# Performance work log

Measured on AMD Instinct MI355X. Metric: run time of the kernel, lower is better.

## Reference

```python
import jax, jax.numpy as jnp
import numpy as np

D_VOCAB, D_MODEL, N_CTX, D_MLP, D_HEAD, N_HEADS, N_LAYERS = 32000, 1024, 2048, 4096, 64, 16, 4
BATCH, SEQ = 2, 2048


def setup_inputs() -> dict:
    key = jax.random.key(0)
    ks = jax.random.split(key, 12)
    sd = 1.0 / np.sqrt(D_MODEL)
    inp = {
        'tokens': jax.random.randint(ks[0], (BATCH, SEQ), 0, D_VOCAB),
        'W_E': jax.random.normal(ks[1], (D_MODEL, D_VOCAB), jnp.float32) * sd,
        'W_pos': jax.random.normal(ks[2], (N_CTX, D_MODEL), jnp.float32) * sd,
        'W_K': jax.random.normal(ks[3], (N_LAYERS, N_HEADS, D_HEAD, D_MODEL), jnp.float32) * sd,
        'W_Q': jax.random.normal(ks[4], (N_LAYERS, N_HEADS, D_HEAD, D_MODEL), jnp.float32) * sd,
        'W_V': jax.random.normal(ks[5], (N_LAYERS, N_HEADS, D_HEAD, D_MODEL), jnp.float32) * sd,
        'W_O': jax.random.normal(ks[6], (N_LAYERS, D_MODEL, D_HEAD * N_HEADS), jnp.float32) * sd,
        'W_in': jax.random.normal(ks[7], (N_LAYERS, D_MLP, D_MODEL), jnp.float32) * sd,
        'b_in': jnp.zeros((N_LAYERS, D_MLP), jnp.float32),
        'W_out': jax.random.normal(ks[8], (N_LAYERS, D_MODEL, D_MLP), jnp.float32) * sd,
        'b_out': jnp.zeros((N_LAYERS, D_MODEL), jnp.float32),
        'W_U': jax.random.normal(ks[9], (D_MODEL, D_VOCAB), jnp.float32) / np.sqrt(D_VOCAB),
    }
    return inp


def reference(tokens, W_E, W_pos, W_K, W_Q, W_V, W_O, W_in, b_in, W_out, b_out, W_U):
    P = tokens.shape[-1]
    # Embed: einsum('dbp->bpd', W_E[:, x])  ==  W_E.T[tokens]
    x = W_E.T[tokens]                      # [b, p, d]
    x = x + W_pos[:P]                      # PosEmbed
    causal = jnp.tril(jnp.ones((P, P), dtype=bool))  # mask[q, p]: p <= q
    scale = 1.0 / np.sqrt(D_HEAD)
    for l in range(N_LAYERS):
        # --- Attention ---
        k = jnp.einsum('ihd,bpd->biph', W_K[l], x)
        q = jnp.einsum('ihd,bpd->biph', W_Q[l], x)
        v = jnp.einsum('ihd,bpd->biph', W_V[l], x)
        scores = jnp.einsum('biph,biqh->biqp', k, q)
        # tril(scores) - 1e10*(1-mask)  ==  where(mask, scores, -1e10)
        masked = jnp.where(causal, scores, jnp.float32(-1e10))
        attn = jax.nn.softmax(masked * scale, axis=-1)   # softmax over keys p
        z = jnp.einsum('biph,biqp->biqh', v, attn)       # [b, i, q, h]
        z_flat = jnp.transpose(z, (0, 2, 1, 3)).reshape(z.shape[0], P, -1)  # b q (i h)
        attn_out = jnp.einsum('df,bqf->bqd', W_O[l], z_flat)
        x = x + attn_out
        # --- MLP (ReLU) ---
        pre = jnp.einsum('md,bpd->bpm', W_in[l], x) + b_in[l]
        post = jax.nn.relu(pre)
        x = x + jnp.einsum('dm,bpm->bpd', W_out[l], post) + b_out[l]
    return x @ W_U                          # logits [b, p, d_vocab]
```

## Files before the change

### kernel.cpp

```cpp
#include <hip/hip_runtime.h>
#include <hip/hip_bf16.h>
#include <math.h>

#define DV   32000
#define DM   1024
#define DMLP 4096
#define DH   64
#define NH   16
#define NL   4
#define BATCH 2
#define S    2048
#define MTOK (BATCH*S)

typedef __bf16 bf16_t;
typedef bf16_t bf16x8 __attribute__((ext_vector_type(8)));
typedef float  f32x4  __attribute__((ext_vector_type(4)));

#define AS1 __attribute__((address_space(1)))
#define AS3 __attribute__((address_space(3)))

__device__ __forceinline__ void gload16(const bf16_t* g, bf16_t* l) {
    __builtin_amdgcn_global_load_lds((const AS1 void*)g, (AS3 void*)l, 16, 0, 0);
}

__device__ __forceinline__ unsigned short bfbits(float v) {
    union { bf16_t b; unsigned short u; } c; c.b = (bf16_t)v; return c.u;
}
__device__ __forceinline__ float b2f(unsigned short u) {
    union { float f; unsigned v; } c; c.v = ((unsigned)u) << 16; return c.f;
}

template<int MODE, bool BIAS, bool RELU>
__global__ __launch_bounds__(256, 2)
void gemm128d(const bf16_t* __restrict__ A, const bf16_t* __restrict__ Bm,
              char* __restrict__ Out, int ldc,
              const float* __restrict__ bias,
              float* __restrict__ resid, bf16_t* __restrict__ residb,
              int K)
{
    const int mb = blockIdx.x, nb = blockIdx.y;

    __shared__ alignas(16) bf16_t lds[2][2][128*64];

    const int tid  = threadIdx.x;
    const int wave = tid >> 6, lane = tid & 63;
    const int wm = wave >> 1, wn = wave & 1;
    const int l16 = lane & 15, lh = lane >> 4;

    const bf16_t* Abase = A  + (long)(mb*128)*K;
    const bf16_t* Bbase = Bm + (long)(nb*128)*K;

    auto stage = [&](int buf, int mat, int k0) {
        const bf16_t* src = (mat ? Bbase : Abase) + k0;
        bf16_t* dst = &lds[buf][mat][0];
#pragma unroll
        for (int u=0; u<4; ++u) {
            int c = u*256 + tid;
            int row = c >> 3, lc = (c & 7) ^ (row & 7);
            gload16(&src[(long)row*K + lc*8], dst + c*8);
        }
    };

    f32x4 acc[4][4];
#pragma unroll
    for (int i=0;i<4;i++)
#pragma unroll
        for (int j=0;j<4;j++) { f32x4 zv={0.f,0.f,0.f,0.f}; acc[i][j]=zv; }

    const int NT = K >> 6;
    stage(0,0,0); stage(0,1,0);

    int cur = 0;
    for (int kt = 0; kt < NT; ++kt) {
        const int nxt = cur ^ 1;
        const int k1 = (kt+1) << 6;
        const bool more = (kt+1 < NT);

        if (more) {
            stage(nxt,0,k1);
            asm volatile("s_waitcnt vmcnt(4)" ::: "memory");
        } else {
            asm volatile("s_waitcnt vmcnt(0)" ::: "memory");
        }
        asm volatile("s_barrier" ::: "memory");

        bf16x8 af[4][2], bfr[4][2];
#pragma unroll
        for (int i=0;i<4;i++) {
            int ra = wm*64 + i*16 + l16;
#pragma unroll
            for (int kk=0;kk<2;kk++)
                af[i][kk] = *(const bf16x8*)&lds[cur][0][ra*64 + (((kk*4+lh)^(ra&7))*8)];
        }
#pragma unroll
        for (int j=0;j<2;j++) {
            int rb = wn*64 + j*16 + l16;
#pragma unroll
            for (int kk=0;kk<2;kk++)
                bfr[j][kk] = *(const bf16x8*)&lds[cur][1][rb*64 + (((kk*4+lh)^(rb&7))*8)];
        }
        __builtin_amdgcn_s_setprio(1);
#pragma unroll
        for (int kk=0;kk<2;kk++)
#pragma unroll
            for (int i=0;i<4;i++)
#pragma unroll
                for (int j=0;j<2;j++)
                    acc[i][j] = __builtin_amdgcn_mfma_f32_16x16x32_bf16(af[i][kk], bfr[j][kk], acc[i][j], 0,0,0);
        __builtin_amdgcn_s_setprio(0);

        if (more) stage(nxt,1,k1);
#pragma unroll
        for (int j=2;j<4;j++) {
            int rb = wn*64 + j*16 + l16;
#pragma unroll
            for (int kk=0;kk<2;kk++)
                bfr[j][kk] = *(const bf16x8*)&lds[cur][1][rb*64 + (((kk*4+lh)^(rb&7))*8)];
        }
        __builtin_amdgcn_s_setprio(1);
#pragma unroll
        for (int kk=0;kk<2;kk++)
#pragma unroll
            for (int i=0;i<4;i++)
#pragma unroll
                for (int j=2;j<4;j++)
                    acc[i][j] = __builtin_amdgcn_mfma_f32_16x16x32_bf16(af[i][kk], bfr[j][kk], acc[i][j], 0,0,0);
        __builtin_amdgcn_s_setprio(0);

        asm volatile("s_barrier" ::: "memory");
        cur = nxt;
    }

    if constexpr (MODE == 1) {
        float* lsl = reinterpret_cast<float*>(&lds[0][0][0]) + wave*(32*68);
        const int lrow = lane >> 4;
        const int lcq  = lane & 15;
#pragma unroll
        for (int ch=0; ch<2; ++ch) {
#pragma unroll
            for (int il=0; il<2; ++il)
#pragma unroll
                for (int j=0;j<4;j++)
#pragma unroll
                    for (int r=0;r<4;r++)
                        lsl[(il*16 + lh*4 + r)*68 + j*16 + l16] = acc[ch*2+il][j][r];
#pragma unroll
            for (int u=0; u<8; ++u) {
                int rl = u*4 + lrow;
                f32x4 v = *(const f32x4*)&lsl[rl*68 + lcq*4];
                long row = mb*128 + wm*64 + ch*32 + rl;
                long col = nb*128 + wn*64 + lcq*4;
                __builtin_nontemporal_store(v, (f32x4*)&((float*)Out)[row*ldc + col]);
            }
        }
    } else {
#pragma unroll
        for (int i=0;i<4;i++) {
            int row0 = mb*128 + wm*64 + i*16 + lh*4;
#pragma unroll
            for (int j=0;j<4;j++) {
                int col = nb*128 + wn*64 + j*16 + l16;
                float bv = BIAS ? bias[col] : 0.0f;
#pragma unroll
                for (int r=0;r<4;r++) {
                    int row = row0 + r;
                    float v = acc[i][j][r] + bv;
                    if (RELU) v = v > 0.f ? v : 0.f;
                    if constexpr (MODE == 0) {
                        ((bf16_t*)Out)[(long)row*ldc + col] = (bf16_t)v;
                    } else {
                        long o2 = (long)row*ldc + col;
                        float nv = resid[o2] + v;
                        resid[o2]  = nv;
                        residb[o2] = (bf16_t)nv;
                    }
                }
            }
        }
    }
}

template<int MODE, bool BIAS, bool RELU>
__global__ __launch_bounds__(512, 1)
void gemm256(const bf16_t* __restrict__ A, const bf16_t* __restrict__ Bm,
             char* __restrict__ Out, int ldc,
             const float* __restrict__ bias, int K)
{
    const int mb = blockIdx.x, nb = blockIdx.y;

    __shared__ alignas(16) bf16_t lds[2][2][2][128*64];

    const int tid  = threadIdx.x;
    const int wave = tid >> 6, lane = tid & 63;
    const int wm = wave >> 2, wn = wave & 3;
    const int l16 = lane & 15, lh = lane >> 4;

    const bf16_t* Abase = A  + (long)(mb*256)*K;
    const bf16_t* Bbase = Bm + (long)(nb*256)*K;

    const int c0 = tid,       r0 = c0 >> 3, lc0 = (c0 & 7) ^ (r0 & 7);
    const int c1 = 512 + tid, r1 = c1 >> 3, lc1 = (c1 & 7) ^ (r1 & 7);

    auto stage = [&](int buf, int mat, int half, int k0) {
        const bf16_t* src = (mat ? Bbase : Abase) + (long)(half*128)*K + k0;
        bf16_t* dst = &lds[buf][mat][half][0];
        gload16(&src[(long)r0*K + lc0*8], dst + c0*8);
        gload16(&src[(long)r1*K + lc1*8], dst + c1*8);
    };

    f32x4 acc[8][4];
#pragma unroll
    for (int i=0;i<8;i++)
#pragma unroll
        for (int j=0;j<4;j++) { f32x4 zv={0.f,0.f,0.f,0.f}; acc[i][j]=zv; }

    const int NT = K >> 6;
    stage(0,0,0,0); stage(0,0,1,0); stage(0,1,0,0); stage(0,1,1,0);

    int cur = 0;
    for (int kt = 0; kt < NT; ++kt) {
        const int nxt = cur ^ 1;
        const int k1 = (kt+1) << 6;
        const bool more = (kt+1 < NT);

        if (more) {
            stage(nxt,0,0,k1);
            asm volatile("s_waitcnt vmcnt(2)" ::: "memory");
        } else {
            asm volatile("s_waitcnt vmcnt(0)" ::: "memory");
        }
        asm volatile("s_barrier" ::: "memory");

        bf16x8 af[4][2], bfr[4][2];
#pragma unroll
        for (int i=0;i<4;i++) {
            int ra = i*16 + l16;
#pragma unroll
            for (int kk=0;kk<2;kk++)
                af[i][kk] = *(const bf16x8*)&lds[cur][0][wm][ra*64 + (((kk*4+lh)^(ra&7))*8)];
        }
#pragma unroll
        for (int j=0;j<2;j++) {
            int rb = (wn&1)*64 + j*16 + l16;
#pragma unroll
            for (int kk=0;kk<2;kk++)
                bfr[j][kk] = *(const bf16x8*)&lds[cur][1][wn>>1][rb*64 + (((kk*4+lh)^(rb&7))*8)];
        }
        __builtin_amdgcn_s_setprio(1);
#pragma unroll
        for (int kk=0;kk<2;kk++)
#pragma unroll
            for (int i=0;i<4;i++)
#pragma unroll
                for (int j=0;j<2;j++)
                    acc[i][j] = __builtin_amdgcn_mfma_f32_16x16x32_bf16(af[i][kk], bfr[j][kk], acc[i][j], 0,0,0);
        __builtin_amdgcn_s_setprio(0);

        if (more) stage(nxt,0,1,k1);
#pragma unroll
        for (int j=2;j<4;j++) {
            int rb = (wn&1)*64 + j*16 + l16;
#pragma unroll
            for (int kk=0;kk<2;kk++)
                bfr[j][kk] = *(const bf16x8*)&lds[cur][1][wn>>1][rb*64 + (((kk*4+lh)^(rb&7))*8)];
        }
        __builtin_amdgcn_s_setprio(1);
#pragma unroll
        for (int kk=0;kk<2;kk++)
#pragma unroll
            for (int i=0;i<4;i++)
#pragma unroll
                for (int j=2;j<4;j++)
                    acc[i][j] = __builtin_amdgcn_mfma_f32_16x16x32_bf16(af[i][kk], bfr[j][kk], acc[i][j], 0,0,0);
        __builtin_amdgcn_s_setprio(0);

        if (more) stage(nxt,1,0,k1);
#pragma unroll
        for (int i=0;i<4;i++) {
            int ra = (i+4)*16 + l16;
#pragma unroll
            for (int kk=0;kk<2;kk++)
                af[i][kk] = *(const bf16x8*)&lds[cur][0][wm][ra*64 + (((kk*4+lh)^(ra&7))*8)];
        }
        __builtin_amdgcn_s_setprio(1);
#pragma unroll
        for (int kk=0;kk<2;kk++)
#pragma unroll
            for (int i=0;i<4;i++)
#pragma unroll
                for (int j=0;j<2;j++)
                    acc[i+4][j] = __builtin_amdgcn_mfma_f32_16x16x32_bf16(af[i][kk], bfr[j][kk], acc[i+4][j], 0,0,0);
        __builtin_amdgcn_s_setprio(0);

        if (more) stage(nxt,1,1,k1);
        __builtin_amdgcn_s_setprio(1);
#pragma unroll
        for (int kk=0;kk<2;kk++)
#pragma unroll
            for (int i=0;i<4;i++)
#pragma unroll
                for (int j=2;j<4;j++)
                    acc[i+4][j] = __builtin_amdgcn_mfma_f32_16x16x32_bf16(af[i][kk], bfr[j][kk], acc[i+4][j], 0,0,0);
        __builtin_amdgcn_s_setprio(0);

        asm volatile("s_barrier" ::: "memory");
        cur = nxt;
    }

#pragma unroll
    for (int i=0;i<8;i++) {
        int row0 = mb*256 + wm*128 + i*16 + lh*4;
#pragma unroll
        for (int j=0;j<4;j++) {
            int col = nb*256 + wn*64 + j*16 + l16;
            float bv = BIAS ? bias[col] : 0.0f;
#pragma unroll
            for (int r=0;r<4;r++) {
                int row = row0 + r;
                float v = acc[i][j][r] + bv;
                if (RELU) v = v > 0.f ? v : 0.f;
                ((bf16_t*)Out)[(long)row*ldc + col] = (bf16_t)v;
            }
        }
    }
}

__global__ __launch_bounds__(256)
void flash_attn(const bf16_t* __restrict__ qkvf,
                const bf16_t* __restrict__ vtg,
                bf16_t* __restrict__ zf)
{
    const int qt = blockIdx.x;
    const int bh = blockIdx.y;
    const int b  = bh >> 4, hd = bh & 15;

    __shared__ alignas(16) bf16_t Kl[64*64];
    __shared__ alignas(16) bf16_t Vtl[64*64];
    __shared__ alignas(16) bf16_t Pl[4*32*64];

    const int tid = threadIdx.x;
    const int wave = tid >> 6, lane = tid & 63;
    const int l16 = lane & 15, lh = lane >> 4;
    const int wq_lo = qt*128 + wave*32;
    bf16_t* Pw = Pl + wave*32*64;

    bf16x8 qr[2][2];
#pragma unroll
    for (int qf=0; qf<2; qf++) {
        int qg = wq_lo + qf*16 + l16;
#pragma unroll
        for (int dhh=0; dhh<2; dhh++)
            qr[qf][dhh] = *(const bf16x8*)&qkvf[((long)b*S + qg)*3072 + hd*64 + dhh*32 + lh*8];
    }

    f32x4 o[4][2];
#pragma unroll
    for (int d=0; d<4; d++)
#pragma unroll
        for (int qf=0; qf<2; qf++) { f32x4 zv={0.f,0.f,0.f,0.f}; o[d][qf]=zv; }
    float mrun[2] = {-1e30f, -1e30f};
    float lrun[2] = {0.f, 0.f};

    const int nt = 2*(qt+1);
    const float C = 0.125f;

    for (int t = 0; t < nt; ++t) {
        const int kv0 = t*64;
        __syncthreads();
#pragma unroll
        for (int u=0; u<2; ++u) {
            int c = u*256 + tid;
            int row = c >> 3, lc = (c & 7) ^ (row & 7);
            gload16(&qkvf[((long)b*S + kv0 + row)*3072 + 1024 + hd*64 + lc*8], &Kl[c*8]);
        }
#pragma unroll
        for (int u=0; u<2; ++u) {
            int c = u*256 + tid;
            int row = c >> 3, lc = (c & 7) ^ (row & 7);
            gload16(&vtg[((long)bh*DH + row)*S + kv0 + lc*8], &Vtl[c*8]);
        }
        __syncthreads();

        f32x4 s[4][2];
#pragma unroll
        for (int f=0; f<4; f++)
#pragma unroll
            for (int qf=0; qf<2; qf++) { f32x4 zv={0.f,0.f,0.f,0.f}; s[f][qf]=zv; }
        __builtin_amdgcn_s_setprio(1);
#pragma unroll
        for (int f=0; f<4; f++) {
            int krow = f*16 + l16;
#pragma unroll
            for (int dhh=0; dhh<2; dhh++) {
                bf16x8 kfr = *(const bf16x8*)&Kl[krow*64 + (((dhh*4+lh) ^ (krow&7))*8)];
#pragma unroll
                for (int qf=0; qf<2; qf++)
                    s[f][qf] = __builtin_amdgcn_mfma_f32_16x16x32_bf16(kfr, qr[qf][dhh], s[f][qf], 0,0,0);
            }
        }
        __builtin_amdgcn_s_setprio(0);

        const bool needmask = (kv0 + 64 > wq_lo);

#pragma unroll
        for (int qf=0; qf<2; qf++) {
            int qg = wq_lo + qf*16 + l16;
            float pmax = -1e30f;
#pragma unroll
            for (int f=0; f<4; f++)
#pragma unroll
                for (int r=0; r<4; r++) {
                    float sv = s[f][qf][r];
                    if (needmask && (kv0 + f*16 + lh*4 + r > qg)) { sv = -1e30f; s[f][qf][r] = sv; }
                    pmax = fmaxf(pmax, sv);
                }
            pmax = fmaxf(pmax, __shfl_xor(pmax, 16));
            pmax = fmaxf(pmax, __shfl_xor(pmax, 32));
            float mnew = fmaxf(mrun[qf], pmax);
            float corr = __expf((mrun[qf] - mnew)*C);
            mrun[qf] = mnew;
            lrun[qf] *= corr;
#pragma unroll
            for (int d=0; d<4; d++) o[d][qf] *= corr;
            float lsum = 0.f;
            int qloc = qf*16 + l16;
#pragma unroll
            for (int f=0; f<4; f++) {
                ushort4 pk;
                float p0 = __expf((s[f][qf][0]-mnew)*C);
                float p1 = __expf((s[f][qf][1]-mnew)*C);
                float p2 = __expf((s[f][qf][2]-mnew)*C);
                float p3 = __expf((s[f][qf][3]-mnew)*C);
                lsum += (p0+p1) + (p2+p3);
                pk.x = bfbits(p0); pk.y = bfbits(p1); pk.z = bfbits(p2); pk.w = bfbits(p3);
                int phys = (f*2 + (lh>>1)) ^ (qloc & 7);
                *(ushort4*)&Pw[qloc*64 + phys*8 + (lh&1)*4] = pk;
            }
            lrun[qf] += lsum;
        }

#pragma unroll
        for (int kh=0; kh<2; kh++) {
            bf16x8 pb[2];
#pragma unroll
            for (int qf=0; qf<2; qf++) {
                int qloc = qf*16 + l16;
                pb[qf] = *(const bf16x8*)&Pw[qloc*64 + (((kh*4+lh) ^ (qloc&7))*8)];
            }
            __builtin_amdgcn_s_setprio(1);
#pragma unroll
            for (int d=0; d<4; d++) {
                int vrow = d*16 + l16;
                bf16x8 va = *(const bf16x8*)&Vtl[vrow*64 + (((kh*4+lh) ^ (vrow&7))*8)];
#pragma unroll
                for (int qf=0; qf<2; qf++)
                    o[d][qf] = __builtin_amdgcn_mfma_f32_16x16x32_bf16(va, pb[qf], o[d][qf], 0,0,0);
            }
            __builtin_amdgcn_s_setprio(0);
        }
    }

#pragma unroll
    for (int qf=0; qf<2; qf++) {
        float lt = lrun[qf];
        lt += __shfl_xor(lt, 16);
        lt += __shfl_xor(lt, 32);
        float inv = 1.0f / lt;
        int qg = wq_lo + qf*16 + l16;
#pragma unroll
        for (int d=0; d<4; d++) {
            ushort4 ov;
            ov.x = bfbits(o[d][qf][0]*inv);
            ov.y = bfbits(o[d][qf][1]*inv);
            ov.z = bfbits(o[d][qf][2]*inv);
            ov.w = bfbits(o[d][qf][3]*inv);
            *(ushort4*)&zf[((long)b*S + qg)*DM + hd*64 + d*16 + lh*4] = ov;
        }
    }
}

__global__ __launch_bounds__(256) void k_conv_qkv(
    const float* __restrict__ Wq, const float* __restrict__ Wk,
    const float* __restrict__ Wv, bf16_t* __restrict__ out)
{
    long idx = ((long)blockIdx.x*256 + threadIdx.x)*4;
    long l = idx / (3072L*DM);
    long r = idx % (3072L*DM);
    int row = (int)(r / DM), d = (int)(r % DM);
    int sel = row >> 10, rr = row & 1023;
    const float* src = sel==0 ? Wq : (sel==1 ? Wk : Wv);
    float4 v = *(const float4*)&src[(l*1024 + rr)*(long)DM + d];
    ushort4 o;
    o.x = bfbits(v.x); o.y = bfbits(v.y); o.z = bfbits(v.z); o.w = bfbits(v.w);
    *(ushort4*)&out[idx] = o;
}

__global__ __launch_bounds__(256) void k_conv(const float* __restrict__ src,
                                              bf16_t* __restrict__ dst, long n)
{
    long i = ((long)blockIdx.x*256 + threadIdx.x)*4;
    if (i >= n) return;
    float4 v = *(const float4*)&src[i];
    ushort4 o;
    o.x = bfbits(v.x); o.y = bfbits(v.y); o.z = bfbits(v.z); o.w = bfbits(v.w);
    *(ushort4*)&dst[i] = o;
}

__global__ __launch_bounds__(256) void k_trans(const float* __restrict__ W,
                                               bf16_t* __restrict__ out, int NC)
{
    __shared__ float tile[32][33];
    int n0 = blockIdx.x*32, k0 = blockIdx.y*32;
    int tx = threadIdx.x & 31, ty = threadIdx.x >> 5;
#pragma unroll
    for (int u=0;u<4;u++)
        tile[ty+u*8][tx] = W[(long)(k0+ty+u*8)*NC + n0+tx];
    __syncthreads();
#pragma unroll
    for (int u=0;u<4;u++)
        out[(long)(n0+ty+u*8)*DM + k0+tx] = (bf16_t)tile[tx][ty+u*8];
}

__global__ __launch_bounds__(256) void k_embed(const int* __restrict__ tok,
    const bf16_t* __restrict__ WEt, const float* __restrict__ Wpos,
    float* __restrict__ xf, bf16_t* __restrict__ xb)
{
    int bp = blockIdx.x;
    int p  = bp & (S-1);
    int t  = tok[bp];
    int d  = threadIdx.x*4;
    ushort4 e = *(const ushort4*)&WEt[(long)t*DM + d];
    float4  w = *(const float4*)&Wpos[(long)p*DM + d];
    float4 v;
    v.x = b2f(e.x)+w.x; v.y = b2f(e.y)+w.y; v.z = b2f(e.z)+w.z; v.w = b2f(e.w)+w.w;
    *(float4*)&xf[(long)bp*DM + d] = v;
    ushort4 o;
    o.x = bfbits(v.x); o.y = bfbits(v.y); o.z = bfbits(v.z); o.w = bfbits(v.w);
    *(ushort4*)&xb[(long)bp*DM + d] = o;
}

__global__ __launch_bounds__(256) void k_permv(const bf16_t* __restrict__ qkv,
    bf16_t* __restrict__ vt)
{
    __shared__ bf16_t tile[64][66];
    const int p0 = blockIdx.x*64;
    const int bh = blockIdx.y;
    const int b  = bh >> 4, hd = bh & 15;
    const int tx = threadIdx.x & 63, ty = threadIdx.x >> 6;
#pragma unroll
    for (int u=0;u<16;u++) {
        int r = u*4 + ty;
        tile[r][tx] = qkv[((long)b*S + p0 + r)*3072 + 2048 + hd*64 + tx];
    }
    __syncthreads();
#pragma unroll
    for (int u=0;u<16;u++) {
        int hh = u*4 + ty;
        vt[(((long)bh)*DH + hh)*S + p0 + tx] = tile[tx][hh];
    }
}

extern "C" void kernel_launch(void* const* d_in, const int* in_sizes, int n_in,
                              void* d_out, int out_size, void* d_ws, size_t ws_size,
                              hipStream_t stream)
{
    const int*   tokens = (const int*)d_in[0];
    const float* W_E    = (const float*)d_in[1];
    const float* W_pos  = (const float*)d_in[2];
    const float* W_K    = (const float*)d_in[3];
    const float* W_Q    = (const float*)d_in[4];
    const float* W_V    = (const float*)d_in[5];
    const float* W_O    = (const float*)d_in[6];
    const float* W_in   = (const float*)d_in[7];
    const float* b_in   = (const float*)d_in[8];
    const float* W_out  = (const float*)d_in[9];
    const float* b_out  = (const float*)d_in[10];
    const float* W_U    = (const float*)d_in[11];
    float* out = (float*)d_out;

    char* ws = (char*)d_ws;
    long off = 0;
    auto alloc = [&](long bytes)->char* {
        char* p = ws + off; off += (bytes + 255) & ~255L; return p;
    };
    bf16_t* wqkv = (bf16_t*)alloc((long)NL*3072*DM*2);
    bf16_t* wo   = (bf16_t*)alloc((long)NL*DM*DM*2);
    bf16_t* win  = (bf16_t*)alloc((long)NL*DMLP*DM*2);
    bf16_t* wout = (bf16_t*)alloc((long)NL*DM*DMLP*2);
    bf16_t* wut  = (bf16_t*)alloc((long)DV*DM*2);
    bf16_t* wet  = (bf16_t*)alloc((long)DV*DM*2);
    float*  xf   = (float*)alloc((long)MTOK*DM*4);
    bf16_t* xb   = (bf16_t*)alloc((long)MTOK*DM*2);
    bf16_t* qkvf = (bf16_t*)alloc((long)MTOK*3072*2);
    bf16_t* vt   = (bf16_t*)alloc((long)BATCH*NH*S*DH*2);
    bf16_t* zf   = (bf16_t*)alloc((long)MTOK*DM*2);
    bf16_t* post = (bf16_t*)alloc((long)MTOK*DMLP*2);

    k_conv_qkv<<<(int)(((long)NL*3072*DM)/1024), 256, 0, stream>>>(W_Q, W_K, W_V, wqkv);
    k_conv<<<(int)(((long)NL*DM*DM)/1024),   256, 0, stream>>>(W_O,   wo,   (long)NL*DM*DM);
    k_conv<<<(int)(((long)NL*DMLP*DM)/1024), 256, 0, stream>>>(W_in,  win,  (long)NL*DMLP*DM);
    k_conv<<<(int)(((long)NL*DM*DMLP)/1024), 256, 0, stream>>>(W_out, wout, (long)NL*DM*DMLP);
    k_trans<<<dim3(DV/32, DM/32), 256, 0, stream>>>(W_U, wut, DV);
    k_trans<<<dim3(DV/32, DM/32), 256, 0, stream>>>(W_E, wet, DV);

    k_embed<<<MTOK, 256, 0, stream>>>(tokens, wet, W_pos, xf, xb);

    for (int l = 0; l < NL; ++l) {
        gemm128d<0,false,false><<<dim3(MTOK/128, 3072/128), 256, 0, stream>>>(
            xb, wqkv + (long)l*3072*DM, (char*)qkvf, 3072, nullptr, nullptr, nullptr, DM);
        k_permv<<<dim3(S/64, BATCH*NH), 256, 0, stream>>>(qkvf, vt);

        flash_attn<<<dim3(S/128, BATCH*NH), 256, 0, stream>>>(qkvf, vt, zf);

        gemm128d<2,false,false><<<dim3(MTOK/128, DM/128), 256, 0, stream>>>(
            zf, wo + (long)l*DM*DM, nullptr, DM, nullptr, xf, xb, DM);
        gemm256<0,true,true><<<dim3(MTOK/256, DMLP/256), 512, 0, stream>>>(
            xb, win + (long)l*DMLP*DM, (char*)post, DMLP,
            b_in + (long)l*DMLP, DM);
        gemm128d<2,true,false><<<dim3(MTOK/128, DM/128), 256, 0, stream>>>(
            post, wout + (long)l*DM*DMLP, nullptr, DM,
            b_out + (long)l*DM, xf, xb, DMLP);
    }

    gemm128d<1,false,false><<<dim3(MTOK/128, DV/128), 256, 0, stream>>>(
        xb, wut, (char*)out, DV, nullptr, nullptr, nullptr, DM);
}
```

Measured before the change: 1.590 ms.

## Double-buffer flash-attention KV loads, swap GEMM tile choices, add LDS-staged fp32 epilogue

Flash attention now double-buffers the K and V tiles in LDS. It issues the next tile's global-to-LDS loads before computing on the current one and waits with vmcnt instead of two __syncthreads per tile. The logits GEMM moves to the 256x256 kernel with a new fp32 epilogue that stages accumulators through LDS and writes coalesced 16-byte nontemporal stores. The MLP up-projection switches from the 256 kernel to the 128 kernel. Together these aim to hide load latency and improve store efficiency on the largest output, at the cost of more LDS per block and changed occupancy.

Result: no change. 1.565 ms (-1.5%).

```diff
diff --git a/kernel.cpp b/kernel.cpp
--- a/kernel.cpp
+++ b/kernel.cpp
@@ -307,19 +307,43 @@
         cur = nxt;
     }
 
-#pragma unroll
-    for (int i=0;i<8;i++) {
-        int row0 = mb*256 + wm*128 + i*16 + lh*4;
-#pragma unroll
-        for (int j=0;j<4;j++) {
-            int col = nb*256 + wn*64 + j*16 + l16;
-            float bv = BIAS ? bias[col] : 0.0f;
-#pragma unroll
-            for (int r=0;r<4;r++) {
-                int row = row0 + r;
-                float v = acc[i][j][r] + bv;
-                if (RELU) v = v > 0.f ? v : 0.f;
-                ((bf16_t*)Out)[(long)row*ldc + col] = (bf16_t)v;
+    if constexpr (MODE == 1) {
+        float* lsl = reinterpret_cast<float*>(&lds[0][0][0][0]) + wave*(32*68);
+        const int lrow = lane >> 4;
+        const int lcq  = lane & 15;
+#pragma unroll
+        for (int ch=0; ch<4; ++ch) {
+#pragma unroll
+            for (int il=0; il<2; ++il)
+#pragma unroll
+                for (int j=0;j<4;j++)
+#pragma unroll
+                    for (int r=0;r<4;r++)
+                        lsl[(il*16 + lh*4 + r)*68 + j*16 + l16] = acc[ch*2+il][j][r];
+#pragma unroll
+            for (int u=0; u<8; ++u) {
+                int rl = u*4 + lrow;
+                f32x4 v = *(const f32x4*)&lsl[rl*68 + lcq*4];
+                long row = mb*256 + wm*128 + ch*32 + rl;
+                long col = nb*256 + wn*64 + lcq*4;
+                __builtin_nontemporal_store(v, (f32x4*)&((float*)Out)[row*ldc + col]);
+            }
+        }
+    } else {
+#pragma unroll
+        for (int i=0;i<8;i++) {
+            int row0 = mb*256 + wm*128 + i*16 + lh*4;
+#pragma unroll
+            for (int j=0;j<4;j++) {
+                int col = nb*256 + wn*64 + j*16 + l16;
+                float bv = BIAS ? bias[col] : 0.0f;
+#pragma unroll
+                for (int r=0;r<4;r++) {
+                    int row = row0 + r;
+                    float v = acc[i][j][r] + bv;
+                    if (RELU) v = v > 0.f ? v : 0.f;
+                    ((bf16_t*)Out)[(long)row*ldc + col] = (bf16_t)v;
+                }
             }
         }
     }
@@ -334,8 +358,8 @@
     const int bh = blockIdx.y;
     const int b  = bh >> 4, hd = bh & 15;
 
-    __shared__ alignas(16) bf16_t Kl[64*64];
-    __shared__ alignas(16) bf16_t Vtl[64*64];
+    __shared__ alignas(16) bf16_t Kl[2][64*64];
+    __shared__ alignas(16) bf16_t Vtl[2][64*64];
     __shared__ alignas(16) bf16_t Pl[4*32*64];
 
     const int tid = threadIdx.x;
@@ -344,6 +368,21 @@
     const int wq_lo = qt*128 + wave*32;
     bf16_t* Pw = Pl + wave*32*64;
 
+    auto stageKV = [&](int buf, int kv0) {
+#pragma unroll
+        for (int u=0; u<2; ++u) {
+            int c = u*256 + tid;
+            int row = c >> 3, lc = (c & 7) ^ (row & 7);
+            gload16(&qkvf[((long)b*S + kv0 + row)*3072 + 1024 + hd*64 + lc*8], &Kl[buf][c*8]);
+        }
+#pragma unroll
+        for (int u=0; u<2; ++u) {
+            int c = u*256 + tid;
+            int row = c >> 3, lc = (c & 7) ^ (row & 7);
+            gload16(&vtg[((long)bh*DH + row)*S + kv0 + lc*8], &Vtl[buf][c*8]);
+        }
+    };
+
     bf16x8 qr[2][2];
 #pragma unroll
     for (int qf=0; qf<2; qf++) {
@@ -364,23 +403,20 @@
     const int nt = 2*(qt+1);
     const float C = 0.125f;
 
+    stageKV(0, 0);
+    int cur = 0;
     for (int t = 0; t < nt; ++t) {
+        const int nxt = cur ^ 1;
+        const bool more = (t+1 < nt);
+        if (more) {
+            stageKV(nxt, (t+1)*64);
+            asm volatile("s_waitcnt vmcnt(4)" ::: "memory");
+        } else {
+            asm volatile("s_waitcnt vmcnt(0)" ::: "memory");
+        }
+        asm volatile("s_barrier" ::: "memory");
+
         const int kv0 = t*64;
-        __syncthreads();
-#pragma unroll
-        for (int u=0; u<2; ++u) {
-            int c = u*256 + tid;
-            int row = c >> 3, lc = (c & 7) ^ (row & 7);
-            gload16(&qkvf[((long)b*S + kv0 + row)*3072 + 1024 + hd*64 + lc*8], &Kl[c*8]);
-        }
-#pragma unroll
-        for (int u=0; u<2; ++u) {
-            int c = u*256 + tid;
-            int row = c >> 3, lc = (c & 7) ^ (row & 7);
-            gload16(&vtg[((long)bh*DH + row)*S + kv0 + lc*8], &Vtl[c*8]);
-        }
-        __syncthreads();
-
         f32x4 s[4][2];
 #pragma unroll
         for (int f=0; f<4; f++)
@@ -392,7 +428,7 @@
             int krow = f*16 + l16;
 #pragma unroll
             for (int dhh=0; dhh<2; dhh++) {
-                bf16x8 kfr = *(const bf16x8*)&Kl[krow*64 + (((dhh*4+lh) ^ (krow&7))*8)];
+                bf16x8 kfr = *(const bf16x8*)&Kl[cur][krow*64 + (((dhh*4+lh) ^ (krow&7))*8)];
 #pragma unroll
                 for (int qf=0; qf<2; qf++)
                     s[f][qf] = __builtin_amdgcn_mfma_f32_16x16x32_bf16(kfr, qr[qf][dhh], s[f][qf], 0,0,0);
@@ -451,13 +487,15 @@
 #pragma unroll
             for (int d=0; d<4; d++) {
                 int vrow = d*16 + l16;
-                bf16x8 va = *(const bf16x8*)&Vtl[vrow*64 + (((kh*4+lh) ^ (vrow&7))*8)];
+                bf16x8 va = *(const bf16x8*)&Vtl[cur][vrow*64 + (((kh*4+lh) ^ (vrow&7))*8)];
 #pragma unroll
                 for (int qf=0; qf<2; qf++)
                     o[d][qf] = __builtin_amdgcn_mfma_f32_16x16x32_bf16(va, pb[qf], o[d][qf], 0,0,0);
             }
             __builtin_amdgcn_s_setprio(0);
         }
+        asm volatile("s_barrier" ::: "memory");
+        cur = nxt;
     }
 
 #pragma unroll
@@ -614,14 +652,14 @@
 
         gemm128d<2,false,false><<<dim3(MTOK/128, DM/128), 256, 0, stream>>>(
             zf, wo + (long)l*DM*DM, nullptr, DM, nullptr, xf, xb, DM);
-        gemm256<0,true,true><<<dim3(MTOK/256, DMLP/256), 512, 0, stream>>>(
+        gemm128d<0,true,true><<<dim3(MTOK/128, DMLP/128), 256, 0, stream>>>(
             xb, win + (long)l*DMLP*DM, (char*)post, DMLP,
-            b_in + (long)l*DMLP, DM);
+            b_in + (long)l*DMLP, nullptr, nullptr, DM);
         gemm128d<2,true,false><<<dim3(MTOK/128, DM/128), 256, 0, stream>>>(
             post, wout + (long)l*DM*DMLP, nullptr, DM,
             b_out + (long)l*DM, xf, xb, DMLP);
     }
 
-    gemm128d<1,false,false><<<dim3(MTOK/128, DV/128), 256, 0, stream>>>(
-        xb, wut, (char*)out, DV, nullptr, nullptr, nullptr, DM);
-}
+    gemm256<1,false,false><<<dim3(MTOK/256, DV/256), 512, 0, stream>>>(
+        xb, wut, (char*)out, DV, nullptr, DM);
+}
```
